# Kernel optimization log

Measured on AMD Instinct MI355X. Metric: run time of the kernel, lower is better.

The kernel has to match this reference:

```python
import jax, jax.numpy as jnp
import numpy as np


def setup_inputs() -> dict:
    key = jax.random.key(0)
    ks = jax.random.split(key, 11)
    b, c, h, w = 16, 64, 16, 16
    F = 64  # num_filters
    O = 64  # num_outputs
    d_in = 2 * (c + 1)  # 130: concat of two (feature + coord) vectors
    s = 0.05
    return {
        "x_img": jax.random.normal(ks[0], (b, c, h, w), dtype=jnp.float32),
        "Wg0": jax.random.normal(ks[1], (F, d_in), dtype=jnp.float32) * s,
        "bg0": jax.random.normal(ks[2], (F,), dtype=jnp.float32) * s,
        "Wg1": jax.random.normal(ks[3], (F, F), dtype=jnp.float32) * s,
        "bg1": jax.random.normal(ks[4], (F,), dtype=jnp.float32) * s,
        "Wg2": jax.random.normal(ks[5], (F, F), dtype=jnp.float32) * s,
        "bg2": jax.random.normal(ks[6], (F,), dtype=jnp.float32) * s,
        "Wp": jax.random.normal(ks[7], (F, F), dtype=jnp.float32) * s,
        "bp": jax.random.normal(ks[8], (F,), dtype=jnp.float32) * s,
        "Wo": jax.random.normal(ks[9], (O, F), dtype=jnp.float32) * s,
        "bo": jax.random.normal(ks[10], (O,), dtype=jnp.float32) * s,
    }


def reference(x_img, Wg0, bg0, Wg1, bg1, Wg2, bg2, Wp, bp, Wo, bo):
    b, c, h, w = x_img.shape
    L = h * w
    # [b, L, c]: flatten spatial, move channels last
    feats = x_img.reshape(b, c, L).transpose(0, 2, 1)
    # append 1-d coordinate feature -> [b, L, c+1]
    coord = jnp.broadcast_to(
        jnp.arange(L, dtype=feats.dtype).reshape(1, L, 1), (b, L, 1)
    )
    feats = jnp.concatenate([feats, coord], axis=2)
    # pairwise broadcast-concat: pair[b, p, q] = [feats[b, q], feats[b, p]]
    d = feats.shape[-1]
    x_i = jnp.broadcast_to(feats[:, None, :, :], (b, L, L, d))
    x_j = jnp.broadcast_to(feats[:, :, None, :], (b, L, L, d))
    pair = jnp.concatenate([x_i, x_j], axis=3)  # [b, L, L, 2*(c+1)]
    # shared g-MLP (3 layers, ReLU)
    out = jax.nn.relu(jnp.einsum("bpqd,fd->bpqf", pair, Wg0) + bg0)
    out = jax.nn.relu(jnp.einsum("bpqf,gf->bpqg", out, Wg1) + bg1)
    out = jax.nn.relu(jnp.einsum("bpqf,gf->bpqg", out, Wg2) + bg2)
    # sum-reduce over both pair dims -> [b, F]
    out = out.sum(axis=(1, 2))
    # f-network
    out = jax.nn.relu(out @ Wp.T + bp)
    out = out @ Wo.T + bo
    return out
```

## Files before the change

### kernel.cpp

```cpp
#include <hip/hip_runtime.h>


typedef short s8v __attribute__((ext_vector_type(8)));
typedef short s4v __attribute__((ext_vector_type(4)));
typedef float f4v __attribute__((ext_vector_type(4)));

#define KEEP(x) asm volatile("" : "+v"(x))

#define MFMA16(a, b, c) __builtin_amdgcn_mfma_f32_16x16x16bf16_1k(a, b, c, 0, 0, 0)

__device__ __forceinline__ short bfr(float v) {
  return __builtin_bit_cast(short, (__bf16)v);
}
__device__ __forceinline__ f4v relu4(f4v v) {
  f4v z = {0.f, 0.f, 0.f, 0.f};
  return __builtin_elementwise_max(v, z);
}
__device__ __forceinline__ s8v cvt8(f4v a, f4v b) {
  s8v r;
  r[0] = bfr(a[0]); r[1] = bfr(a[1]); r[2] = bfr(a[2]); r[3] = bfr(a[3]);
  r[4] = bfr(b[0]); r[5] = bfr(b[1]); r[6] = bfr(b[2]); r[7] = bfr(b[3]);
  return r;
}
__device__ __forceinline__ s4v cvt4(f4v a) {
  s4v r;
  r[0] = bfr(a[0]); r[1] = bfr(a[1]); r[2] = bfr(a[2]); r[3] = bfr(a[3]);
  return r;
}
__device__ __forceinline__ f4v ldf4(const float* p) {
  return *(const f4v*)p;
}

__global__ __launch_bounds__(256) void k_pre(
    const float* __restrict__ x, const float* __restrict__ Wg0,
    const float* __restrict__ bg0, float* __restrict__ Ag,
    float* __restrict__ Bg) {
  __shared__ float ws[64 * 131];
  __shared__ float xs[64 * 17];

  const int t = threadIdx.x;
  const int b = blockIdx.x >> 4;
  const int l0 = (blockIdx.x & 15) * 16;

  for (int i = t; i < 64 * 130; i += 256) {
    int f = i / 130, d = i - f * 130;
    ws[f * 131 + d] = Wg0[i];
  }
  for (int i = t; i < 64 * 16; i += 256) {
    int ch = i >> 4, li = i & 15;
    xs[ch * 17 + li] = x[b * 16384 + ch * 256 + l0 + li];
  }
  __syncthreads();

  const int f = t & 63;
  const int w = t >> 6;
  float accA[4] = {0.f, 0.f, 0.f, 0.f};
  float accB[4] = {0.f, 0.f, 0.f, 0.f};
  for (int d = 0; d < 64; ++d) {
    float wa = ws[f * 131 + d];
    float wb = ws[f * 131 + 65 + d];
#pragma unroll
    for (int i = 0; i < 4; ++i) {
      float xv = xs[d * 17 + w + 4 * i];
      accA[i] += xv * wa;
      accB[i] += xv * wb;
    }
  }
  const float wca = ws[f * 131 + 64];
  const float wcb = ws[f * 131 + 129];
  const float bias = bg0[f];
#pragma unroll
  for (int i = 0; i < 4; ++i) {
    int l = l0 + w + 4 * i;
    Ag[(b * 256 + l) * 64 + f] = accA[i] + (float)l * wca;
    Bg[(b * 256 + l) * 64 + f] = accB[i] + (float)l * wcb + bias;
  }
}

__global__ __launch_bounds__(256, 2) void k_main(
    const float* __restrict__ Ag, const float* __restrict__ Bg,
    const float* __restrict__ Wg1, const float* __restrict__ bg1,
    const float* __restrict__ Wg2, const float* __restrict__ bg2,
    float* __restrict__ Part) {
  __shared__ __align__(16) float Bs[32 * 64];
  __shared__ float Sblk[64];

  const int t = threadIdx.x;
  const int wid = t >> 6;
  const int lane = t & 63;
  const int mm = lane & 15;
  const int quad = lane >> 4;
  const int b = blockIdx.y;
  const int blkx = blockIdx.x;
  const int qq = blkx & 3;
  const int p0 = (blkx >> 2) * 32;
  const int q0 = (qq * 4 + wid) * 16;

  if (t < 64) Sblk[t] = 0.f;

  {
    const f4v* Bb4 = (const f4v*)(Bg + (b * 256 + p0) * 64);
    ((f4v*)Bs)[t] = Bb4[t];
    ((f4v*)Bs)[t + 256] = Bb4[t + 256];
  }

  const float* Arow = Ag + (b * 256 + q0 + mm) * 64;
  f4v af0 = ldf4(Arow + quad * 8);
  f4v af1 = ldf4(Arow + quad * 8 + 4);
  f4v af2 = ldf4(Arow + 32 + quad * 8);
  f4v af3 = ldf4(Arow + 36 + quad * 8);

  s8v W1f[4][2];
  s4v W2f[4][4];
  f4v c1i[4], c2i[4];
#pragma unroll
  for (int gt = 0; gt < 4; ++gt) {
    c1i[gt] = ldf4(bg1 + gt * 16 + quad * 4);
    c2i[gt] = ldf4(bg2 + gt * 16 + quad * 4);
#pragma unroll
    for (int kh = 0; kh < 2; ++kh) {
      const float* r1 = Wg1 + (gt * 16 + mm) * 64 + kh * 32 + quad * 8;
      W1f[gt][kh] = cvt8(ldf4(r1), ldf4(r1 + 4));
    }
#pragma unroll
    for (int kt = 0; kt < 4; ++kt) {
      const float* r2 = Wg2 + (gt * 16 + mm) * 64 + kt * 16 + quad * 4;
      W2f[gt][kt] = cvt4(ldf4(r2));
    }
  }
#pragma unroll
  for (int gt = 0; gt < 4; ++gt) {
    KEEP(W1f[gt][0]); KEEP(W1f[gt][1]);
    KEEP(W2f[gt][0]); KEEP(W2f[gt][1]); KEEP(W2f[gt][2]); KEEP(W2f[gt][3]);
    KEEP(c1i[gt]); KEEP(c2i[gt]);
  }
  KEEP(af0); KEEP(af1); KEEP(af2); KEEP(af3);

  __syncthreads();

  f4v cs[4] = {{0.f,0.f,0.f,0.f},{0.f,0.f,0.f,0.f},
               {0.f,0.f,0.f,0.f},{0.f,0.f,0.f,0.f}};

  f4v bq0 = ldf4(Bs + quad * 8);
  f4v bq1 = ldf4(Bs + quad * 8 + 4);
  f4v bq2 = ldf4(Bs + 32 + quad * 8);
  f4v bq3 = ldf4(Bs + 36 + quad * 8);

  for (int ip = 0; ip < 32; ++ip) {
    const float* bn = Bs + ((ip < 31) ? ip + 1 : 31) * 64;
    f4v bn0 = ldf4(bn + quad * 8);
    f4v bn1 = ldf4(bn + quad * 8 + 4);
    f4v bn2 = ldf4(bn + 32 + quad * 8);
    f4v bn3 = ldf4(bn + 36 + quad * 8);

    s8v x0 = cvt8(relu4(af0 + bq0), relu4(af1 + bq1));
    s8v x1 = cvt8(relu4(af2 + bq2), relu4(af3 + bq3));

    s4v pk[4];
#pragma unroll
    for (int gt = 0; gt < 4; ++gt) {
      f4v a = c1i[gt];
      a = __builtin_amdgcn_mfma_f32_16x16x32_bf16(W1f[gt][0], x0, a, 0, 0, 0);
      a = __builtin_amdgcn_mfma_f32_16x16x32_bf16(W1f[gt][1], x1, a, 0, 0, 0);
      pk[gt] = cvt4(relu4(a));
    }
#pragma unroll
    for (int ot = 0; ot < 4; ++ot) {
      f4v a = c2i[ot];
      a = MFMA16(W2f[ot][0], pk[0], a);
      a = MFMA16(W2f[ot][1], pk[1], a);
      a = MFMA16(W2f[ot][2], pk[2], a);
      a = MFMA16(W2f[ot][3], pk[3], a);
      cs[ot] += relu4(a);
    }

    bq0 = bn0; bq1 = bn1; bq2 = bn2; bq3 = bn3;
  }

#pragma unroll
  for (int ot = 0; ot < 4; ++ot) {
#pragma unroll
    for (int r = 0; r < 4; ++r) {
      float v = cs[ot][r];
      v += __shfl_xor(v, 1);
      v += __shfl_xor(v, 2);
      v += __shfl_xor(v, 4);
      v += __shfl_xor(v, 8);
      if (mm == 0) atomicAdd(&Sblk[ot * 16 + quad * 4 + r], v);
    }
  }
  __syncthreads();
  if (t < 64) Part[(b * 32 + blkx) * 64 + t] = Sblk[t];
}

__global__ __launch_bounds__(64) void k_final(
    const float* __restrict__ Part, const float* __restrict__ Wp,
    const float* __restrict__ bp, const float* __restrict__ Wo,
    const float* __restrict__ bo, float* __restrict__ out) {
  __shared__ float sv[64], tv[64];
  const int b = blockIdx.x, t = threadIdx.x;
  float s = 0.f;
  const float* Pb = Part + b * 32 * 64;
#pragma unroll
  for (int j = 0; j < 32; ++j) s += Pb[j * 64 + t];
  sv[t] = s;
  __syncthreads();
  float acc = bp[t];
  for (int g = 0; g < 64; ++g) acc += sv[g] * Wp[t * 64 + g];
  tv[t] = fmaxf(acc, 0.f);
  __syncthreads();
  float o = bo[t];
  for (int f = 0; f < 64; ++f) o += tv[f] * Wo[t * 64 + f];
  out[b * 64 + t] = o;
}

extern "C" void kernel_launch(void* const* d_in, const int* in_sizes, int n_in,
                              void* d_out, int out_size, void* d_ws, size_t ws_size,
                              hipStream_t stream) {
  const float* x   = (const float*)d_in[0];
  const float* Wg0 = (const float*)d_in[1];
  const float* bg0 = (const float*)d_in[2];
  const float* Wg1 = (const float*)d_in[3];
  const float* bg1 = (const float*)d_in[4];
  const float* Wg2 = (const float*)d_in[5];
  const float* bg2 = (const float*)d_in[6];
  const float* Wp  = (const float*)d_in[7];
  const float* bp  = (const float*)d_in[8];
  const float* Wo  = (const float*)d_in[9];
  const float* bo  = (const float*)d_in[10];
  float* out = (float*)d_out;

  float* Ag   = (float*)d_ws;
  float* Bg   = Ag + 16 * 256 * 64;
  float* Part = Bg + 16 * 256 * 64;

  k_pre<<<256, 256, 0, stream>>>(x, Wg0, bg0, Ag, Bg);
  k_main<<<dim3(32, 16), 256, 0, stream>>>(Ag, Bg, Wg1, bg1, Wg2, bg2, Part);
  k_final<<<16, 64, 0, stream>>>(Part, Wp, bp, Wo, bo, out);
}
```

Measured before the change: 113.3 us.

## Fuse three kernels into one cooperative kernel with grid syncs

```diff
diff --git a/kernel.cpp b/kernel.cpp
--- a/kernel.cpp
+++ b/kernel.cpp
@@ -1,4 +1,7 @@
 #include <hip/hip_runtime.h>
+#include <hip/hip_cooperative_groups.h>
+
+namespace cg = cooperative_groups;
 
 
 typedef short s8v __attribute__((ext_vector_type(8)));
@@ -29,6 +32,208 @@
 }
 __device__ __forceinline__ f4v ldf4(const float* p) {
   return *(const f4v*)p;
+}
+
+__global__ __launch_bounds__(256, 2) void k_fused(
+    const float* __restrict__ x, const float* __restrict__ Wg0,
+    const float* __restrict__ bg0, const float* __restrict__ Wg1,
+    const float* __restrict__ bg1, const float* __restrict__ Wg2,
+    const float* __restrict__ bg2, const float* __restrict__ Wp,
+    const float* __restrict__ bp, const float* __restrict__ Wo,
+    const float* __restrict__ bo, float* __restrict__ out,
+    float* __restrict__ Ag, float* __restrict__ Bg,
+    float* __restrict__ Part) {
+  __shared__ __align__(16) float LDS[8960];
+  const int t = threadIdx.x;
+  const int bx = blockIdx.x;
+  const int by = blockIdx.y;
+  cg::grid_group grid = cg::this_grid();
+
+  {
+    float* ws = LDS;
+    float* xs = LDS + 8384;
+    const int b = by, l0 = bx * 8;
+    for (int i = t; i < 64 * 130; i += 256) {
+      int f = i / 130, d = i - f * 130;
+      ws[f * 131 + d] = Wg0[i];
+    }
+    for (int i = t; i < 512; i += 256) {
+      int ch = i >> 3, li = i & 7;
+      xs[ch * 9 + li] = x[b * 16384 + ch * 256 + l0 + li];
+    }
+    __syncthreads();
+    const int f = t & 63;
+    const int w = t >> 6;
+    float aA0 = 0.f, aA1 = 0.f, aB0 = 0.f, aB1 = 0.f;
+    for (int d = 0; d < 64; ++d) {
+      float wa = ws[f * 131 + d];
+      float wb = ws[f * 131 + 65 + d];
+      float x0 = xs[d * 9 + w];
+      float x1 = xs[d * 9 + w + 4];
+      aA0 += x0 * wa; aA1 += x1 * wa;
+      aB0 += x0 * wb; aB1 += x1 * wb;
+    }
+    const float wca = ws[f * 131 + 64];
+    const float wcb = ws[f * 131 + 129];
+    const float bias = bg0[f];
+    const int la = l0 + w, lb = l0 + w + 4;
+    Ag[(b * 256 + la) * 64 + f] = aA0 + (float)la * wca;
+    Bg[(b * 256 + la) * 64 + f] = aB0 + (float)la * wcb + bias;
+    Ag[(b * 256 + lb) * 64 + f] = aA1 + (float)lb * wca;
+    Bg[(b * 256 + lb) * 64 + f] = aB1 + (float)lb * wcb + bias;
+  }
+  __threadfence();
+  grid.sync();
+
+  {
+    float* Bs = LDS;
+    float* WaveS = LDS + 2048;
+    const int wid = t >> 6;
+    const int lane = t & 63;
+    const int mm = lane & 15;
+    const int quad = lane >> 4;
+    const int b = by;
+    const int blkx = bx;
+    const int qq = blkx & 3;
+    const int p0 = (blkx >> 2) * 32;
+    const int q0 = (qq * 4 + wid) * 16;
+
+    {
+      const f4v* Bb4 = (const f4v*)(Bg + (b * 256 + p0) * 64);
+      ((f4v*)Bs)[t] = Bb4[t];
+      ((f4v*)Bs)[t + 256] = Bb4[t + 256];
+    }
+
+    const float* Arow = Ag + (b * 256 + q0 + mm) * 64;
+    f4v af0 = ldf4(Arow + quad * 8);
+    f4v af1 = ldf4(Arow + quad * 8 + 4);
+    f4v af2 = ldf4(Arow + 32 + quad * 8);
+    f4v af3 = ldf4(Arow + 36 + quad * 8);
+
+    s8v W1f[4][2];
+    s4v W2f[4][4];
+    f4v c1i[4], c2i[4];
+#pragma unroll
+    for (int gt = 0; gt < 4; ++gt) {
+      c1i[gt] = ldf4(bg1 + gt * 16 + quad * 4);
+      c2i[gt] = ldf4(bg2 + gt * 16 + quad * 4);
+#pragma unroll
+      for (int kh = 0; kh < 2; ++kh) {
+        const float* r1 = Wg1 + (gt * 16 + mm) * 64 + kh * 32 + quad * 8;
+        W1f[gt][kh] = cvt8(ldf4(r1), ldf4(r1 + 4));
+      }
+#pragma unroll
+      for (int kt = 0; kt < 4; ++kt) {
+        const float* r2 = Wg2 + (gt * 16 + mm) * 64 + kt * 16 + quad * 4;
+        W2f[gt][kt] = cvt4(ldf4(r2));
+      }
+    }
+#pragma unroll
+    for (int gt = 0; gt < 4; ++gt) {
+      KEEP(W1f[gt][0]); KEEP(W1f[gt][1]);
+      KEEP(W2f[gt][0]); KEEP(W2f[gt][1]); KEEP(W2f[gt][2]); KEEP(W2f[gt][3]);
+      KEEP(c1i[gt]); KEEP(c2i[gt]);
+    }
+    KEEP(af0); KEEP(af1); KEEP(af2); KEEP(af3);
+
+    __syncthreads();
+
+    f4v cs[4] = {{0.f,0.f,0.f,0.f},{0.f,0.f,0.f,0.f},
+                 {0.f,0.f,0.f,0.f},{0.f,0.f,0.f,0.f}};
+
+    f4v bq0 = ldf4(Bs + quad * 8);
+    f4v bq1 = ldf4(Bs + quad * 8 + 4);
+    f4v bq2 = ldf4(Bs + 32 + quad * 8);
+    f4v bq3 = ldf4(Bs + 36 + quad * 8);
+
+    for (int ip = 0; ip < 32; ++ip) {
+      const float* bn = Bs + ((ip < 31) ? ip + 1 : 31) * 64;
+      f4v bn0 = ldf4(bn + quad * 8);
+      f4v bn1 = ldf4(bn + quad * 8 + 4);
+      f4v bn2 = ldf4(bn + 32 + quad * 8);
+      f4v bn3 = ldf4(bn + 36 + quad * 8);
+
+      s8v x0 = cvt8(relu4(af0 + bq0), relu4(af1 + bq1));
+      s8v x1 = cvt8(relu4(af2 + bq2), relu4(af3 + bq3));
+
+      s4v pk[4];
+#pragma unroll
+      for (int gt = 0; gt < 4; ++gt) {
+        f4v a = c1i[gt];
+        a = __builtin_amdgcn_mfma_f32_16x16x32_bf16(W1f[gt][0], x0, a, 0, 0, 0);
+        a = __builtin_amdgcn_mfma_f32_16x16x32_bf16(W1f[gt][1], x1, a, 0, 0, 0);
+        pk[gt] = cvt4(relu4(a));
+      }
+#pragma unroll
+      for (int ot = 0; ot < 4; ++ot) {
+        f4v a = c2i[ot];
+        a = MFMA16(W2f[ot][0], pk[0], a);
+        a = MFMA16(W2f[ot][1], pk[1], a);
+        a = MFMA16(W2f[ot][2], pk[2], a);
+        a = MFMA16(W2f[ot][3], pk[3], a);
+        cs[ot] += relu4(a);
+      }
+
+      bq0 = bn0; bq1 = bn1; bq2 = bn2; bq3 = bn3;
+    }
+
+#pragma unroll
+    for (int ot = 0; ot < 4; ++ot) {
+#pragma unroll
+      for (int r = 0; r < 4; ++r) {
+        float v = cs[ot][r];
+        v += __shfl_xor(v, 1);
+        v += __shfl_xor(v, 2);
+        v += __shfl_xor(v, 4);
+        v += __shfl_xor(v, 8);
+        if (mm == 0) WaveS[wid * 64 + ot * 16 + quad * 4 + r] = v;
+      }
+    }
+    __syncthreads();
+    if (t < 64) {
+      float s = WaveS[t] + WaveS[64 + t] + WaveS[128 + t] + WaveS[192 + t];
+      Part[(b * 32 + blkx) * 64 + t] = s;
+    }
+  }
+  __threadfence();
+  grid.sync();
+
+  if (by == 0 && bx < 16) {
+    const int b = bx;
+    const int o = t & 63, jw = t >> 6;
+    float s = 0.f;
+    const float* Pb = Part + b * 2048;
+#pragma unroll
+    for (int j = 0; j < 8; ++j) s += Pb[(jw * 8 + j) * 64 + o];
+    LDS[jw * 64 + o] = s;
+    __syncthreads();
+    if (t < 64) {
+      float sum = LDS[t] + LDS[64 + t] + LDS[128 + t] + LDS[192 + t];
+      LDS[256 + t] = sum;
+    }
+    __syncthreads();
+    if (t < 64) {
+      float acc = bp[t];
+#pragma unroll
+      for (int g4 = 0; g4 < 16; ++g4) {
+        f4v wv = ldf4(Wp + t * 64 + g4 * 4);
+        f4v xv = ldf4(&LDS[256 + g4 * 4]);
+        acc += wv[0] * xv[0] + wv[1] * xv[1] + wv[2] * xv[2] + wv[3] * xv[3];
+      }
+      LDS[320 + t] = fmaxf(acc, 0.f);
+    }
+    __syncthreads();
+    if (t < 64) {
+      float o2 = bo[t];
+#pragma unroll
+      for (int g4 = 0; g4 < 16; ++g4) {
+        f4v wv = ldf4(Wo + t * 64 + g4 * 4);
+        f4v xv = ldf4(&LDS[320 + g4 * 4]);
+        o2 += wv[0] * xv[0] + wv[1] * xv[1] + wv[2] * xv[2] + wv[3] * xv[3];
+      }
+      out[b * 64 + t] = o2;
+    }
+  }
 }
 
 __global__ __launch_bounds__(256) void k_pre(
@@ -83,7 +288,7 @@
     const float* __restrict__ Wg2, const float* __restrict__ bg2,
     float* __restrict__ Part) {
   __shared__ __align__(16) float Bs[32 * 64];
-  __shared__ float Sblk[64];
+  __shared__ float WaveS[4 * 64];
 
   const int t = threadIdx.x;
   const int wid = t >> 6;
@@ -96,8 +301,6 @@
   const int p0 = (blkx >> 2) * 32;
   const int q0 = (qq * 4 + wid) * 16;
 
-  if (t < 64) Sblk[t] = 0.f;
-
   {
     const f4v* Bb4 = (const f4v*)(Bg + (b * 256 + p0) * 64);
     ((f4v*)Bs)[t] = Bb4[t];
@@ -186,11 +389,14 @@
       v += __shfl_xor(v, 2);
       v += __shfl_xor(v, 4);
       v += __shfl_xor(v, 8);
-      if (mm == 0) atomicAdd(&Sblk[ot * 16 + quad * 4 + r], v);
+      if (mm == 0) WaveS[wid * 64 + ot * 16 + quad * 4 + r] = v;
     }
   }
   __syncthreads();
-  if (t < 64) Part[(b * 32 + blkx) * 64 + t] = Sblk[t];
+  if (t < 64) {
+    float s = WaveS[t] + WaveS[64 + t] + WaveS[128 + t] + WaveS[192 + t];
+    Part[(b * 32 + blkx) * 64 + t] = s;
+  }
 }
 
 __global__ __launch_bounds__(64) void k_final(
@@ -234,7 +440,16 @@
   float* Bg   = Ag + 16 * 256 * 64;
   float* Part = Bg + 16 * 256 * 64;
 
-  k_pre<<<256, 256, 0, stream>>>(x, Wg0, bg0, Ag, Bg);
-  k_main<<<dim3(32, 16), 256, 0, stream>>>(Ag, Bg, Wg1, bg1, Wg2, bg2, Part);
-  k_final<<<16, 64, 0, stream>>>(Part, Wp, bp, Wo, bo, out);
-}
+  void* args[] = {
+      (void*)&x,  (void*)&Wg0, (void*)&bg0, (void*)&Wg1, (void*)&bg1,
+      (void*)&Wg2, (void*)&bg2, (void*)&Wp, (void*)&bp, (void*)&Wo,
+      (void*)&bo, (void*)&out, (void*)&Ag, (void*)&Bg, (void*)&Part};
+  hipError_t err = hipLaunchCooperativeKernel(
+      (const void*)k_fused, dim3(32, 16, 1), dim3(256, 1, 1), (void**)args, 0,
+      stream);
+  if (err != hipSuccess) {
+    k_pre<<<256, 256, 0, stream>>>(x, Wg0, bg0, Ag, Bg);
+    k_main<<<dim3(32, 16), 256, 0, stream>>>(Ag, Bg, Wg1, bg1, Wg2, bg2, Part);
+    k_final<<<16, 64, 0, stream>>>(Part, Wp, bp, Wo, bo, out);
+  }
+}
```

Result: slower. 268.6 us (+137.0%).

## Halve per-block pair tile, double grid, replace LDS atomics with per-wave slots

Applied to the files above, without the earlier changes.

```diff
diff --git a/kernel.cpp b/kernel.cpp
--- a/kernel.cpp
+++ b/kernel.cpp
@@ -77,13 +77,13 @@
   }
 }
 
-__global__ __launch_bounds__(256, 2) void k_main(
+__global__ __launch_bounds__(256, 4) void k_main(
     const float* __restrict__ Ag, const float* __restrict__ Bg,
     const float* __restrict__ Wg1, const float* __restrict__ bg1,
     const float* __restrict__ Wg2, const float* __restrict__ bg2,
     float* __restrict__ Part) {
-  __shared__ __align__(16) float Bs[32 * 64];
-  __shared__ float Sblk[64];
+  __shared__ __align__(16) float Bs[16 * 64];
+  __shared__ float WaveS[4 * 64];
 
   const int t = threadIdx.x;
   const int wid = t >> 6;
@@ -93,15 +93,12 @@
   const int b = blockIdx.y;
   const int blkx = blockIdx.x;
   const int qq = blkx & 3;
-  const int p0 = (blkx >> 2) * 32;
+  const int p0 = (blkx >> 2) * 16;
   const int q0 = (qq * 4 + wid) * 16;
-
-  if (t < 64) Sblk[t] = 0.f;
 
   {
     const f4v* Bb4 = (const f4v*)(Bg + (b * 256 + p0) * 64);
     ((f4v*)Bs)[t] = Bb4[t];
-    ((f4v*)Bs)[t + 256] = Bb4[t + 256];
   }
 
   const float* Arow = Ag + (b * 256 + q0 + mm) * 64;
@@ -146,8 +143,8 @@
   f4v bq2 = ldf4(Bs + 32 + quad * 8);
   f4v bq3 = ldf4(Bs + 36 + quad * 8);
 
-  for (int ip = 0; ip < 32; ++ip) {
-    const float* bn = Bs + ((ip < 31) ? ip + 1 : 31) * 64;
+  for (int ip = 0; ip < 16; ++ip) {
+    const float* bn = Bs + ((ip < 15) ? ip + 1 : 15) * 64;
     f4v bn0 = ldf4(bn + quad * 8);
     f4v bn1 = ldf4(bn + quad * 8 + 4);
     f4v bn2 = ldf4(bn + 32 + quad * 8);
@@ -186,32 +183,53 @@
       v += __shfl_xor(v, 2);
       v += __shfl_xor(v, 4);
       v += __shfl_xor(v, 8);
-      if (mm == 0) atomicAdd(&Sblk[ot * 16 + quad * 4 + r], v);
-    }
-  }
-  __syncthreads();
-  if (t < 64) Part[(b * 32 + blkx) * 64 + t] = Sblk[t];
-}
-
-__global__ __launch_bounds__(64) void k_final(
+      if (mm == 0) WaveS[wid * 64 + ot * 16 + quad * 4 + r] = v;
+    }
+  }
+  __syncthreads();
+  if (t < 64) {
+    float s = WaveS[t] + WaveS[64 + t] + WaveS[128 + t] + WaveS[192 + t];
+    Part[(b * 64 + blkx) * 64 + t] = s;
+  }
+}
+
+__global__ __launch_bounds__(256) void k_final(
     const float* __restrict__ Part, const float* __restrict__ Wp,
     const float* __restrict__ bp, const float* __restrict__ Wo,
     const float* __restrict__ bo, float* __restrict__ out) {
+  __shared__ float red[4][64];
   __shared__ float sv[64], tv[64];
   const int b = blockIdx.x, t = threadIdx.x;
+  const int o = t & 63, jw = t >> 6;
+  const float* Pb = Part + b * 64 * 64;
   float s = 0.f;
-  const float* Pb = Part + b * 32 * 64;
-#pragma unroll
-  for (int j = 0; j < 32; ++j) s += Pb[j * 64 + t];
-  sv[t] = s;
-  __syncthreads();
-  float acc = bp[t];
-  for (int g = 0; g < 64; ++g) acc += sv[g] * Wp[t * 64 + g];
-  tv[t] = fmaxf(acc, 0.f);
-  __syncthreads();
-  float o = bo[t];
-  for (int f = 0; f < 64; ++f) o += tv[f] * Wo[t * 64 + f];
-  out[b * 64 + t] = o;
+#pragma unroll
+  for (int j = 0; j < 16; ++j) s += Pb[(jw * 16 + j) * 64 + o];
+  red[jw][o] = s;
+  __syncthreads();
+  if (t < 64) sv[t] = red[0][t] + red[1][t] + red[2][t] + red[3][t];
+  __syncthreads();
+  if (t < 64) {
+    float acc = bp[t];
+#pragma unroll
+    for (int g4 = 0; g4 < 16; ++g4) {
+      f4v wv = ldf4(Wp + t * 64 + g4 * 4);
+      f4v xv = ldf4(sv + g4 * 4);
+      acc += wv[0] * xv[0] + wv[1] * xv[1] + wv[2] * xv[2] + wv[3] * xv[3];
+    }
+    tv[t] = fmaxf(acc, 0.f);
+  }
+  __syncthreads();
+  if (t < 64) {
+    float o2 = bo[t];
+#pragma unroll
+    for (int g4 = 0; g4 < 16; ++g4) {
+      f4v wv = ldf4(Wo + t * 64 + g4 * 4);
+      f4v xv = ldf4(tv + g4 * 4);
+      o2 += wv[0] * xv[0] + wv[1] * xv[1] + wv[2] * xv[2] + wv[3] * xv[3];
+    }
+    out[b * 64 + t] = o2;
+  }
 }
 
 extern "C" void kernel_launch(void* const* d_in, const int* in_sizes, int n_in,
@@ -235,6 +253,6 @@
   float* Part = Bg + 16 * 256 * 64;
 
   k_pre<<<256, 256, 0, stream>>>(x, Wg0, bg0, Ag, Bg);
-  k_main<<<dim3(32, 16), 256, 0, stream>>>(Ag, Bg, Wg1, bg1, Wg2, bg2, Part);
-  k_final<<<16, 64, 0, stream>>>(Part, Wp, bp, Wo, bo, out);
-}
+  k_main<<<dim3(64, 16), 256, 0, stream>>>(Ag, Bg, Wg1, bg1, Wg2, bg2, Part);
+  k_final<<<16, 256, 0, stream>>>(Part, Wp, bp, Wo, bo, out);
+}
```

New measurement: 172.4 us. +52.1%, slower.
